# Kernel tuning notes

Hardware: AMD Instinct MI355X
Metric: run time of the kernel (lower is better)

Reference implementation:

```python
import jax, jax.numpy as jnp
import numpy as np

EMBED = 1024
HEADS = 16
HEAD_DIM = EMBED // HEADS


def setup_inputs() -> dict:
    key = jax.random.key(0)
    ks = jax.random.split(key, 5)
    s = 1.0 / np.sqrt(EMBED)
    return {
        "x": jax.random.normal(ks[0], (4, 2048, EMBED), dtype=jnp.float32),
        "W_qkv": jax.random.uniform(ks[1], (EMBED, 3 * EMBED), jnp.float32, -s, s),
        "b_qkv": jax.random.uniform(ks[2], (3 * EMBED,), jnp.float32, -s, s),
        "W_out": jax.random.uniform(ks[3], (EMBED, EMBED), jnp.float32, -s, s),
        "b_out": jax.random.uniform(ks[4], (EMBED,), jnp.float32, -s, s),
    }


def reference(x, W_qkv, b_qkv, W_out, b_out):
    B, S, E = x.shape
    qkv = x @ W_qkv + b_qkv  # [B,S,3E]
    q, k, v = jnp.split(qkv, 3, axis=-1)
    # [B,S,E] -> [B,H,S,D]
    def split_heads(t):
        return t.reshape(B, S, HEADS, HEAD_DIM).transpose(0, 2, 1, 3)
    q, k, v = split_heads(q), split_heads(k), split_heads(v)
    scale = 1.0 / jnp.sqrt(jnp.asarray(HEAD_DIM, dtype=x.dtype))
    scores = jnp.einsum("bhqd,bhkd->bhqk", q, k) * scale
    attn = jax.nn.softmax(scores, axis=-1)
    out = jnp.einsum("bhqk,bhkd->bhqd", attn, v)
    out = out.transpose(0, 2, 1, 3).reshape(B, S, E)
    return out @ W_out + b_out
```

## Files before the change

### kernel.cpp

```cpp
#include <hip/hip_runtime.h>
#include <hip/hip_bf16.h>

typedef __bf16 bf16;
typedef __bf16 bf16x8 __attribute__((ext_vector_type(8)));
typedef float f32x4 __attribute__((ext_vector_type(4)));
typedef float f32x16 __attribute__((ext_vector_type(16)));

#define EMB 1024
#define SEQ 2048
#define NH 16
#define HD 64
#define MTOK 8192

__global__ __launch_bounds__(256) void cast_f32_bf16(const float* __restrict__ in,
                                                     bf16* __restrict__ out, int n8) {
    int i = blockIdx.x * blockDim.x + threadIdx.x;
    if (i < n8) {
        const float4* p = (const float4*)in + 2 * (size_t)i;
        float4 a = p[0], b = p[1];
        bf16x8 v;
        v[0] = (bf16)a.x; v[1] = (bf16)a.y; v[2] = (bf16)a.z; v[3] = (bf16)a.w;
        v[4] = (bf16)b.x; v[5] = (bf16)b.y; v[6] = (bf16)b.z; v[7] = (bf16)b.w;
        *(bf16x8*)(out + 8 * (size_t)i) = v;
    }
}

__global__ __launch_bounds__(256) void transpose_cast(const float* __restrict__ W,
                                                      bf16* __restrict__ Wt, int K, int N) {
    __shared__ float tile[32][33];
    int n0 = blockIdx.x * 32, k0 = blockIdx.y * 32;
    int tx = threadIdx.x & 31, ty = threadIdx.x >> 5;
    #pragma unroll
    for (int i = 0; i < 32; i += 8)
        tile[ty + i][tx] = W[(size_t)(k0 + ty + i) * N + n0 + tx];
    __syncthreads();
    #pragma unroll
    for (int i = 0; i < 32; i += 8)
        Wt[(size_t)(n0 + ty + i) * K + k0 + tx] = (bf16)tile[tx][ty + i];
}

#define BM 128
#define BN 128
#define BK 64
#define LDK 72

#define QSCALE 0.1803368801111f

__global__ __launch_bounds__(256) void gemm_qkv(const bf16* __restrict__ A,
                                                const bf16* __restrict__ Bt,
                                                const float* __restrict__ bias,
                                                bf16* __restrict__ qws, bf16* __restrict__ kws,
                                                bf16* __restrict__ vt) {
    __shared__ bf16 sA[BM][LDK];
    __shared__ bf16 sB[BN][LDK];
    const int K = 1024;
    int m0 = blockIdx.x * BM, n0 = blockIdx.y * BN;
    int t = threadIdx.x, lane = t & 63, w = t >> 6;
    int wr = w >> 1, wc = w & 1;
    int l15 = lane & 15, quad = lane >> 4;

    f32x4 acc[4][4];
    #pragma unroll
    for (int i = 0; i < 4; i++)
        #pragma unroll
        for (int j = 0; j < 4; j++) acc[i][j] = (f32x4){0.f, 0.f, 0.f, 0.f};

    int srow = t >> 3, sc8 = (t & 7) * 8;
    for (int kt = 0; kt < K; kt += BK) {
        #pragma unroll
        for (int p = 0; p < 4; p++) {
            int r = srow + p * 32;
            *(uint4*)&sA[r][sc8] = *(const uint4*)(A + (size_t)(m0 + r) * K + kt + sc8);
            *(uint4*)&sB[r][sc8] = *(const uint4*)(Bt + (size_t)(n0 + r) * K + kt + sc8);
        }
        __syncthreads();
        #pragma unroll
        for (int ks = 0; ks < BK; ks += 32) {
            int kk = ks + quad * 8;
            bf16x8 af[4], bfr[4];
            #pragma unroll
            for (int mt = 0; mt < 4; mt++) af[mt] = *(const bf16x8*)&sA[wr * 64 + mt * 16 + l15][kk];
            #pragma unroll
            for (int nt = 0; nt < 4; nt++) bfr[nt] = *(const bf16x8*)&sB[wc * 64 + nt * 16 + l15][kk];
            #pragma unroll
            for (int mt = 0; mt < 4; mt++)
                #pragma unroll
                for (int nt = 0; nt < 4; nt++)
                    acc[mt][nt] = __builtin_amdgcn_mfma_f32_16x16x32_bf16(af[mt], bfr[nt], acc[mt][nt], 0, 0, 0);
        }
        __syncthreads();
    }
    #pragma unroll
    for (int mt = 0; mt < 4; mt++)
        #pragma unroll
        for (int nt = 0; nt < 4; nt++) {
            int col = n0 + wc * 64 + nt * 16 + l15;
            float bv = bias[col];
            int mat = col >> 10;
            int e = col & 1023;
            int h = e >> 6, d = e & 63;
            int row0 = m0 + wr * 64 + mt * 16 + quad * 4;
            int bb = row0 >> 11, s0 = row0 & 2047;
            int bh = bb * NH + h;
            float vv[4];
            #pragma unroll
            for (int r = 0; r < 4; r++) vv[r] = acc[mt][nt][r] + bv;
            if (mat == 0) {
                #pragma unroll
                for (int r = 0; r < 4; r++)
                    qws[((size_t)bh * SEQ + s0 + r) * HD + d] = (bf16)(vv[r] * QSCALE);
            } else if (mat == 1) {
                #pragma unroll
                for (int r = 0; r < 4; r++)
                    kws[((size_t)bh * SEQ + s0 + r) * HD + d] = (bf16)vv[r];
            } else {
                ushort4 pk;
                pk.x = __builtin_bit_cast(unsigned short, (bf16)vv[0]);
                pk.y = __builtin_bit_cast(unsigned short, (bf16)vv[1]);
                pk.z = __builtin_bit_cast(unsigned short, (bf16)vv[2]);
                pk.w = __builtin_bit_cast(unsigned short, (bf16)vv[3]);
                *(ushort4*)((unsigned short*)vt + ((size_t)bh * HD + d) * SEQ + s0) = pk;
            }
        }
}

__device__ __forceinline__ unsigned pk2(float a, float b) {
    unsigned lo = (unsigned)__builtin_bit_cast(unsigned short, (bf16)a);
    unsigned hi = (unsigned)__builtin_bit_cast(unsigned short, (bf16)b);
    return lo | (hi << 16);
}

__global__ __launch_bounds__(256) void attn(const bf16* __restrict__ qws, const bf16* __restrict__ kws,
                                            const bf16* __restrict__ vt, bf16* __restrict__ ao) {
    __shared__ bf16 sK[64][72];
    __shared__ bf16 sVt[64][72];

    int q0 = blockIdx.x * 256, bh = blockIdx.y;
    int t = threadIdx.x, lane = t & 63, w = t >> 6;
    int l31 = lane & 31, hi = lane >> 5;

    const bf16* qb = qws + (size_t)bh * SEQ * HD;
    const bf16* kb = kws + (size_t)bh * SEQ * HD;
    const bf16* vtb = vt + (size_t)bh * HD * SEQ;

    bf16x8 qf[2][4];
    #pragma unroll
    for (int nq = 0; nq < 2; nq++)
        #pragma unroll
        for (int ks = 0; ks < 4; ks++)
            qf[nq][ks] = *(const bf16x8*)(qb + (size_t)(q0 + w * 64 + nq * 32 + l31) * HD + ks * 16 + hi * 8);

    f32x16 o[2][2];
    float lsum[2] = {0.f, 0.f};
    #pragma unroll
    for (int mt = 0; mt < 2; mt++)
        #pragma unroll
        for (int nq = 0; nq < 2; nq++)
            #pragma unroll
            for (int r = 0; r < 16; r++) o[mt][nq][r] = 0.f;

    int krow = t >> 3, kc8 = (t & 7) * 8;
    int vdr = t >> 2, vc16 = (t & 3) * 16;

    for (int kv0 = 0; kv0 < SEQ; kv0 += 64) {
        #pragma unroll
        for (int p = 0; p < 2; p++) {
            int r = krow + p * 32;
            *(uint4*)&sK[r][kc8] = *(const uint4*)(kb + (size_t)(kv0 + r) * HD + kc8);
        }
        {
            const bf16* src = vtb + (size_t)vdr * SEQ + kv0 + vc16;
            *(uint4*)&sVt[vdr][vc16] = *(const uint4*)src;
            *(uint4*)&sVt[vdr][vc16 + 8] = *(const uint4*)(src + 8);
        }
        __syncthreads();

        f32x16 sacc[2][2];
        #pragma unroll
        for (int nt = 0; nt < 2; nt++)
            #pragma unroll
            for (int nq = 0; nq < 2; nq++)
                #pragma unroll
                for (int r = 0; r < 16; r++) sacc[nt][nq][r] = 0.f;
        #pragma unroll
        for (int ks = 0; ks < 4; ks++)
            #pragma unroll
            for (int nt = 0; nt < 2; nt++) {
                bf16x8 kf = *(const bf16x8*)&sK[nt * 32 + l31][ks * 16 + hi * 8];
                #pragma unroll
                for (int nq = 0; nq < 2; nq++)
                    sacc[nt][nq] = __builtin_amdgcn_mfma_f32_32x32x16_bf16(kf, qf[nq][ks], sacc[nt][nq], 0, 0, 0);
            }

        bf16x8 pb[2][4];
        #pragma unroll
        for (int nt = 0; nt < 2; nt++)
            #pragma unroll
            for (int nq = 0; nq < 2; nq++) {
                float e[16];
                #pragma unroll
                for (int r = 0; r < 16; r++) {
                    e[r] = __builtin_amdgcn_exp2f(sacc[nt][nq][r]);
                    lsum[nq] += e[r];
                }
                #pragma unroll
                for (int blk = 0; blk < 2; blk++) {
                    int b = blk * 8;
                    unsigned x0 = pk2(e[b + 0], e[b + 1]), x1 = pk2(e[b + 2], e[b + 3]);
                    unsigned y0 = pk2(e[b + 4], e[b + 5]), y1 = pk2(e[b + 6], e[b + 7]);
                    unsigned r0 = __shfl_xor(hi ? x0 : y0, 32);
                    unsigned r1 = __shfl_xor(hi ? x1 : y1, 32);
                    uint4 f;
                    f.x = hi ? r0 : x0;
                    f.y = hi ? r1 : x1;
                    f.z = hi ? y0 : r0;
                    f.w = hi ? y1 : r1;
                    pb[nq][nt * 2 + blk] = __builtin_bit_cast(bf16x8, f);
                }
            }

        #pragma unroll
        for (int s = 0; s < 4; s++)
            #pragma unroll
            for (int mt = 0; mt < 2; mt++) {
                bf16x8 vf = *(const bf16x8*)&sVt[mt * 32 + l31][s * 16 + hi * 8];
                #pragma unroll
                for (int nq = 0; nq < 2; nq++)
                    o[mt][nq] = __builtin_amdgcn_mfma_f32_32x32x16_bf16(vf, pb[nq][s], o[mt][nq], 0, 0, 0);
            }
        __syncthreads();
    }

    float inv[2];
    #pragma unroll
    for (int nq = 0; nq < 2; nq++) {
        float s = lsum[nq] + __shfl_xor(lsum[nq], 32);
        inv[nq] = __builtin_amdgcn_rcpf(s);
    }

    int h = bh & 15, bb = bh >> 4;
    #pragma unroll
    for (int mt = 0; mt < 2; mt++)
        #pragma unroll
        for (int nq = 0; nq < 2; nq++) {
            int q = q0 + w * 64 + nq * 32 + l31;
            #pragma unroll
            for (int g = 0; g < 4; g++) {
                ushort4 pk;
                pk.x = __builtin_bit_cast(unsigned short, (bf16)(o[mt][nq][4 * g + 0] * inv[nq]));
                pk.y = __builtin_bit_cast(unsigned short, (bf16)(o[mt][nq][4 * g + 1] * inv[nq]));
                pk.z = __builtin_bit_cast(unsigned short, (bf16)(o[mt][nq][4 * g + 2] * inv[nq]));
                pk.w = __builtin_bit_cast(unsigned short, (bf16)(o[mt][nq][4 * g + 3] * inv[nq]));
                *(ushort4*)((unsigned short*)ao + ((size_t)(bb * SEQ + q)) * EMB + h * HD + mt * 32 + 8 * g + 4 * hi) = pk;
            }
        }
}

__global__ __launch_bounds__(256) void gemm_out(const bf16* __restrict__ A,
                                                const bf16* __restrict__ Bt,
                                                const float* __restrict__ bias,
                                                float* __restrict__ out) {
    __shared__ bf16 sA[BM][LDK];
    __shared__ bf16 sB[BN][LDK];
    const int K = 1024;
    int m0 = blockIdx.x * BM, n0 = blockIdx.y * BN;
    int t = threadIdx.x, lane = t & 63, w = t >> 6;
    int wr = w >> 1, wc = w & 1;
    int l15 = lane & 15, quad = lane >> 4;

    f32x4 acc[4][4];
    #pragma unroll
    for (int i = 0; i < 4; i++)
        #pragma unroll
        for (int j = 0; j < 4; j++) acc[i][j] = (f32x4){0.f, 0.f, 0.f, 0.f};

    int srow = t >> 3, sc8 = (t & 7) * 8;
    for (int kt = 0; kt < K; kt += BK) {
        #pragma unroll
        for (int p = 0; p < 4; p++) {
            int r = srow + p * 32;
            *(uint4*)&sA[r][sc8] = *(const uint4*)(A + (size_t)(m0 + r) * K + kt + sc8);
            *(uint4*)&sB[r][sc8] = *(const uint4*)(Bt + (size_t)(n0 + r) * K + kt + sc8);
        }
        __syncthreads();
        #pragma unroll
        for (int ks = 0; ks < BK; ks += 32) {
            int kk = ks + quad * 8;
            bf16x8 af[4], bfr[4];
            #pragma unroll
            for (int mt = 0; mt < 4; mt++) af[mt] = *(const bf16x8*)&sA[wr * 64 + mt * 16 + l15][kk];
            #pragma unroll
            for (int nt = 0; nt < 4; nt++) bfr[nt] = *(const bf16x8*)&sB[wc * 64 + nt * 16 + l15][kk];
            #pragma unroll
            for (int mt = 0; mt < 4; mt++)
                #pragma unroll
                for (int nt = 0; nt < 4; nt++)
                    acc[mt][nt] = __builtin_amdgcn_mfma_f32_16x16x32_bf16(af[mt], bfr[nt], acc[mt][nt], 0, 0, 0);
        }
        __syncthreads();
    }
    #pragma unroll
    for (int mt = 0; mt < 4; mt++)
        #pragma unroll
        for (int nt = 0; nt < 4; nt++) {
            int col = n0 + wc * 64 + nt * 16 + l15;
            float bv = bias[col];
            #pragma unroll
            for (int r = 0; r < 4; r++) {
                int row = m0 + wr * 64 + mt * 16 + quad * 4 + r;
                out[(size_t)row * EMB + col] = acc[mt][nt][r] + bv;
            }
        }
}

extern "C" void kernel_launch(void* const* d_in, const int* in_sizes, int n_in,
                              void* d_out, int out_size, void* d_ws, size_t ws_size,
                              hipStream_t stream) {
    const float* x     = (const float*)d_in[0];
    const float* W_qkv = (const float*)d_in[1];
    const float* b_qkv = (const float*)d_in[2];
    const float* W_out = (const float*)d_in[3];
    const float* b_out = (const float*)d_in[4];
    float* out = (float*)d_out;

    char* ws = (char*)d_ws;
    bf16* xb    = (bf16*)(ws);
    bf16* wqkvT = (bf16*)(ws + (size_t)(16 << 20));
    bf16* woutT = (bf16*)(ws + (size_t)(22 << 20));
    bf16* qws   = (bf16*)(ws + (size_t)(24 << 20));
    bf16* kws   = (bf16*)(ws + (size_t)(40 << 20));
    bf16* vt    = (bf16*)(ws + (size_t)(56 << 20));
    bf16* aow   = (bf16*)(ws + (size_t)(72 << 20));

    cast_f32_bf16<<<4096, 256, 0, stream>>>(x, xb, MTOK * EMB / 8);
    transpose_cast<<<dim3(3 * EMB / 32, EMB / 32), 256, 0, stream>>>(W_qkv, wqkvT, EMB, 3 * EMB);
    transpose_cast<<<dim3(EMB / 32, EMB / 32), 256, 0, stream>>>(W_out, woutT, EMB, EMB);
    gemm_qkv<<<dim3(MTOK / BM, 3 * EMB / BN), 256, 0, stream>>>(xb, wqkvT, b_qkv, qws, kws, vt);
    attn<<<dim3(SEQ / 256, 64), 256, 0, stream>>>(qws, kws, vt, aow);
    gemm_out<<<dim3(MTOK / BM, EMB / BN), 256, 0, stream>>>(aow, woutT, b_out, out);
}
```

Baseline: 307.9 us.

## Halve attention query tile per wave and use permlane32 swap for P repack

Each attention block now covers 128 queries instead of 256, and each wave handles 32 query rows instead of 64. This doubles the grid to 1024 blocks and roughly halves per-thread accumulator registers, which should raise occupancy. The exp/bf16 repack replaces the shfl_xor and select sequence with v_permlane32_swap_b32 inline asm to exchange halves across the 32-lane boundary. The cost is that K/V tiles are loaded into shared memory twice as often per query, so there is less reuse per LDS load.

```diff
diff --git a/kernel.cpp b/kernel.cpp
--- a/kernel.cpp
+++ b/kernel.cpp
@@ -135,7 +135,7 @@
     __shared__ bf16 sK[64][72];
     __shared__ bf16 sVt[64][72];
 
-    int q0 = blockIdx.x * 256, bh = blockIdx.y;
+    int q0 = blockIdx.x * 128, bh = blockIdx.y;
     int t = threadIdx.x, lane = t & 63, w = t >> 6;
     int l31 = lane & 31, hi = lane >> 5;
 
@@ -143,21 +143,17 @@
     const bf16* kb = kws + (size_t)bh * SEQ * HD;
     const bf16* vtb = vt + (size_t)bh * HD * SEQ;
 
-    bf16x8 qf[2][4];
-    #pragma unroll
-    for (int nq = 0; nq < 2; nq++)
-        #pragma unroll
-        for (int ks = 0; ks < 4; ks++)
-            qf[nq][ks] = *(const bf16x8*)(qb + (size_t)(q0 + w * 64 + nq * 32 + l31) * HD + ks * 16 + hi * 8);
-
-    f32x16 o[2][2];
-    float lsum[2] = {0.f, 0.f};
+    bf16x8 qf[4];
+    #pragma unroll
+    for (int ks = 0; ks < 4; ks++)
+        qf[ks] = *(const bf16x8*)(qb + (size_t)(q0 + w * 32 + l31) * HD + ks * 16 + hi * 8);
+
+    f32x16 o[2];
+    float lsum = 0.f;
     #pragma unroll
     for (int mt = 0; mt < 2; mt++)
         #pragma unroll
-        for (int nq = 0; nq < 2; nq++)
-            #pragma unroll
-            for (int r = 0; r < 16; r++) o[mt][nq][r] = 0.f;
+        for (int r = 0; r < 16; r++) o[mt][r] = 0.f;
 
     int krow = t >> 3, kc8 = (t & 7) * 8;
     int vdr = t >> 2, vc16 = (t & 3) * 16;
@@ -175,84 +171,67 @@
         }
         __syncthreads();
 
-        f32x16 sacc[2][2];
+        f32x16 sacc[2];
         #pragma unroll
         for (int nt = 0; nt < 2; nt++)
             #pragma unroll
-            for (int nq = 0; nq < 2; nq++)
-                #pragma unroll
-                for (int r = 0; r < 16; r++) sacc[nt][nq][r] = 0.f;
+            for (int r = 0; r < 16; r++) sacc[nt][r] = 0.f;
         #pragma unroll
         for (int ks = 0; ks < 4; ks++)
             #pragma unroll
             for (int nt = 0; nt < 2; nt++) {
                 bf16x8 kf = *(const bf16x8*)&sK[nt * 32 + l31][ks * 16 + hi * 8];
-                #pragma unroll
-                for (int nq = 0; nq < 2; nq++)
-                    sacc[nt][nq] = __builtin_amdgcn_mfma_f32_32x32x16_bf16(kf, qf[nq][ks], sacc[nt][nq], 0, 0, 0);
-            }
-
-        bf16x8 pb[2][4];
-        #pragma unroll
-        for (int nt = 0; nt < 2; nt++)
-            #pragma unroll
-            for (int nq = 0; nq < 2; nq++) {
-                float e[16];
-                #pragma unroll
-                for (int r = 0; r < 16; r++) {
-                    e[r] = __builtin_amdgcn_exp2f(sacc[nt][nq][r]);
-                    lsum[nq] += e[r];
-                }
-                #pragma unroll
-                for (int blk = 0; blk < 2; blk++) {
-                    int b = blk * 8;
-                    unsigned x0 = pk2(e[b + 0], e[b + 1]), x1 = pk2(e[b + 2], e[b + 3]);
-                    unsigned y0 = pk2(e[b + 4], e[b + 5]), y1 = pk2(e[b + 6], e[b + 7]);
-                    unsigned r0 = __shfl_xor(hi ? x0 : y0, 32);
-                    unsigned r1 = __shfl_xor(hi ? x1 : y1, 32);
-                    uint4 f;
-                    f.x = hi ? r0 : x0;
-                    f.y = hi ? r1 : x1;
-                    f.z = hi ? y0 : r0;
-                    f.w = hi ? y1 : r1;
-                    pb[nq][nt * 2 + blk] = __builtin_bit_cast(bf16x8, f);
-                }
-            }
+                sacc[nt] = __builtin_amdgcn_mfma_f32_32x32x16_bf16(kf, qf[ks], sacc[nt], 0, 0, 0);
+            }
+
+        bf16x8 pb[4];
+        #pragma unroll
+        for (int nt = 0; nt < 2; nt++) {
+            float e[16];
+            #pragma unroll
+            for (int r = 0; r < 16; r++) {
+                e[r] = __builtin_amdgcn_exp2f(sacc[nt][r]);
+                lsum += e[r];
+            }
+            #pragma unroll
+            for (int blk = 0; blk < 2; blk++) {
+                int b = blk * 8;
+                unsigned a0 = pk2(e[b + 0], e[b + 1]);
+                unsigned a1 = pk2(e[b + 2], e[b + 3]);
+                unsigned b0 = pk2(e[b + 4], e[b + 5]);
+                unsigned b1 = pk2(e[b + 6], e[b + 7]);
+                asm("v_permlane32_swap_b32 %0, %1" : "+v"(a0), "+v"(b0));
+                asm("v_permlane32_swap_b32 %0, %1" : "+v"(a1), "+v"(b1));
+                uint4 f;
+                f.x = a0; f.y = a1; f.z = b0; f.w = b1;
+                pb[nt * 2 + blk] = __builtin_bit_cast(bf16x8, f);
+            }
+        }
 
         #pragma unroll
         for (int s = 0; s < 4; s++)
             #pragma unroll
             for (int mt = 0; mt < 2; mt++) {
                 bf16x8 vf = *(const bf16x8*)&sVt[mt * 32 + l31][s * 16 + hi * 8];
-                #pragma unroll
-                for (int nq = 0; nq < 2; nq++)
-                    o[mt][nq] = __builtin_amdgcn_mfma_f32_32x32x16_bf16(vf, pb[nq][s], o[mt][nq], 0, 0, 0);
+                o[mt] = __builtin_amdgcn_mfma_f32_32x32x16_bf16(vf, pb[s], o[mt], 0, 0, 0);
             }
         __syncthreads();
     }
 
-    float inv[2];
-    #pragma unroll
-    for (int nq = 0; nq < 2; nq++) {
-        float s = lsum[nq] + __shfl_xor(lsum[nq], 32);
-        inv[nq] = __builtin_amdgcn_rcpf(s);
-    }
+    float inv = __builtin_amdgcn_rcpf(lsum + __shfl_xor(lsum, 32));
 
     int h = bh & 15, bb = bh >> 4;
+    int q = q0 + w * 32 + l31;
     #pragma unroll
     for (int mt = 0; mt < 2; mt++)
         #pragma unroll
-        for (int nq = 0; nq < 2; nq++) {
-            int q = q0 + w * 64 + nq * 32 + l31;
-            #pragma unroll
-            for (int g = 0; g < 4; g++) {
-                ushort4 pk;
-                pk.x = __builtin_bit_cast(unsigned short, (bf16)(o[mt][nq][4 * g + 0] * inv[nq]));
-                pk.y = __builtin_bit_cast(unsigned short, (bf16)(o[mt][nq][4 * g + 1] * inv[nq]));
-                pk.z = __builtin_bit_cast(unsigned short, (bf16)(o[mt][nq][4 * g + 2] * inv[nq]));
-                pk.w = __builtin_bit_cast(unsigned short, (bf16)(o[mt][nq][4 * g + 3] * inv[nq]));
-                *(ushort4*)((unsigned short*)ao + ((size_t)(bb * SEQ + q)) * EMB + h * HD + mt * 32 + 8 * g + 4 * hi) = pk;
-            }
+        for (int g = 0; g < 4; g++) {
+            ushort4 pk;
+            pk.x = __builtin_bit_cast(unsigned short, (bf16)(o[mt][4 * g + 0] * inv));
+            pk.y = __builtin_bit_cast(unsigned short, (bf16)(o[mt][4 * g + 1] * inv));
+            pk.z = __builtin_bit_cast(unsigned short, (bf16)(o[mt][4 * g + 2] * inv));
+            pk.w = __builtin_bit_cast(unsigned short, (bf16)(o[mt][4 * g + 3] * inv));
+            *(ushort4*)((unsigned short*)ao + ((size_t)(bb * SEQ + q)) * EMB + h * HD + mt * 32 + 8 * g + 4 * hi) = pk;
         }
 }
 
@@ -336,6 +315,6 @@
     transpose_cast<<<dim3(3 * EMB / 32, EMB / 32), 256, 0, stream>>>(W_qkv, wqkvT, EMB, 3 * EMB);
     transpose_cast<<<dim3(EMB / 32, EMB / 32), 256, 0, stream>>>(W_out, woutT, EMB, EMB);
     gemm_qkv<<<dim3(MTOK / BM, 3 * EMB / BN), 256, 0, stream>>>(xb, wqkvT, b_qkv, qws, kws, vt);
-    attn<<<dim3(SEQ / 256, 64), 256, 0, stream>>>(qws, kws, vt, aow);
+    attn<<<dim3(SEQ / 128, 64), 256, 0, stream>>>(qws, kws, vt, aow);
     gemm_out<<<dim3(MTOK / BM, EMB / BN), 256, 0, stream>>>(aow, woutT, b_out, out);
 }
```

Measured after the change: 288.4 us. 1.07x faster.
